# Kernel tuning notes

Measured on AMD Instinct MI355X. Metric: run time of the kernel, lower is better.

## Reference

```python
import jax, jax.numpy as jnp
import numpy as np

N = 100000          # nodes
E = 3200000         # edges (avg degree 32)
IN = 128            # input_dim
H = 16              # hidden1 == hidden2 (GENConv out channels)
OUT = 32            # output_dim
EDGE_DIM = 8        # edge_feature_dim (unused: conv called with edge_attr=None)
MSG_EPS = 1e-7      # GENConv message eps
BN_EPS = 1e-5       # BatchNorm1d eps
T = 1.0             # softmax aggregation temperature


def setup_inputs() -> dict:
    key = jax.random.key(0)
    ks = jax.random.split(key, 24)
    s = lambda fan: 1.0 / np.sqrt(fan)
    inp = {
        "num_nodes": N,
        "edge_index": jax.random.randint(ks[0], (2, E), 0, N, dtype=jnp.int64),
        "edge_attr": jax.random.normal(ks[1], (E, EDGE_DIM), dtype=jnp.float32),
        "x": jax.random.normal(ks[2], (N, IN), dtype=jnp.float32),
        "node_mask": (jnp.arange(N) % 2).astype(jnp.int32),  # exactly N//2 nonzero
        # conv1 lin_src (in != out -> projection)
        "W_src": jax.random.normal(ks[3], (IN, H), dtype=jnp.float32) * s(IN),
        "b_src": jnp.zeros((H,), dtype=jnp.float32),
        # conv1 MLP: [H, 2H, H] with BatchNorm+ReLU between
        "c1_W1": jax.random.normal(ks[4], (H, 2 * H), dtype=jnp.float32) * s(H),
        "c1_b1": jnp.zeros((2 * H,), dtype=jnp.float32),
        "c1_g": jnp.ones((2 * H,), dtype=jnp.float32),
        "c1_be": jnp.zeros((2 * H,), dtype=jnp.float32),
        "c1_W2": jax.random.normal(ks[5], (2 * H, H), dtype=jnp.float32) * s(2 * H),
        "c1_b2": jnp.zeros((H,), dtype=jnp.float32),
        # conv2 MLP (in == out -> no lin_src)
        "c2_W1": jax.random.normal(ks[6], (H, 2 * H), dtype=jnp.float32) * s(H),
        "c2_b1": jnp.zeros((2 * H,), dtype=jnp.float32),
        "c2_g": jnp.ones((2 * H,), dtype=jnp.float32),
        "c2_be": jnp.zeros((2 * H,), dtype=jnp.float32),
        "c2_W2": jax.random.normal(ks[7], (2 * H, H), dtype=jnp.float32) * s(2 * H),
        "c2_b2": jnp.zeros((H,), dtype=jnp.float32),
        # final fc
        "fc_W": jax.random.normal(ks[8], (H, OUT), dtype=jnp.float32) * s(H),
        "fc_b": jnp.zeros((OUT,), dtype=jnp.float32),
    }
    return inp


def _softmax_aggregate(msg, dst, n):
    # per-destination, per-channel softmax-weighted sum (PyG softmax aggr, t=T)
    m = jax.ops.segment_max(msg * T, dst, num_segments=n)          # [n, C]
    ex = jnp.exp(msg * T - m[dst])                                  # [E, C]
    denom = jax.ops.segment_sum(ex, dst, num_segments=n)           # [n, C]
    alpha = ex / denom[dst]
    return jax.ops.segment_sum(alpha * msg, dst, num_segments=n)


def _genconv(x, src, dst, n, lin, mlp):
    if lin is not None:
        x = x @ lin[0] + lin[1]                                     # lin_src projection
    msg = jax.nn.relu(x[src]) + MSG_EPS                             # message (edge_attr=None)
    aggr = _softmax_aggregate(msg, dst, n)
    h = aggr + x                                                    # residual add of x_r
    W1, b1, g, be, W2, b2 = mlp
    h = h @ W1 + b1
    mu = h.mean(axis=0)
    var = h.var(axis=0)                                             # biased var (torch BN)
    h = (h - mu) * jax.lax.rsqrt(var + BN_EPS) * g + be
    return jax.nn.relu(h) @ W2 + b2


def reference(num_nodes, edge_index, edge_attr, x, node_mask,
              W_src, b_src,
              c1_W1, c1_b1, c1_g, c1_be, c1_W2, c1_b2,
              c2_W1, c2_b1, c2_g, c2_be, c2_W2, c2_b2,
              fc_W, fc_b):
    src, dst = edge_index[0], edge_index[1]
    h = _genconv(x, src, dst, num_nodes, (W_src, b_src),
                 (c1_W1, c1_b1, c1_g, c1_be, c1_W2, c1_b2))
    h = jax.nn.relu(h)
    h = _genconv(h, src, dst, num_nodes, None,
                 (c2_W1, c2_b1, c2_g, c2_be, c2_W2, c2_b2))
    h = jax.nn.relu(h)
    out = h @ fc_W + fc_b
    # mask has exactly N//2 nonzeros by construction -> static-size nonzero
    idx = jnp.nonzero(node_mask != 0, size=node_mask.shape[0] // 2)[0]
    return out[idx]
```

## Files before the change

kernel.cpp:

```cpp
#include <hip/hip_runtime.h>

#define NN 100000
#define NE 3200000
#define NB 391
#define NBIN3 782
#define BINW3 128
#define BCAP3 4608
#define BIN_BLOCKS 512
#define CHUNK 6250
#define AGGR4_BLOCKS 1563

static_assert(NB * 256 >= NN, "NB");
static_assert(NBIN3 * BINW3 >= NN, "BINW3");
static_assert(BIN_BLOCKS * CHUNK == NE, "CHUNK");
static_assert(AGGR4_BLOCKS * 256 >= NN * 4, "AGGR4");

__device__ __forceinline__ int wave_incl_scan_i(int v) {
#pragma unroll
  for (int off = 1; off < 64; off <<= 1) {
    int n = __shfl_up(v, off);
    if ((int)(threadIdx.x & 63) >= off) v += n;
  }
  return v;
}

__global__ __launch_bounds__(256) void k_hist(const int* __restrict__ ei,
                                              int* __restrict__ hcnt) {
  __shared__ int hist[NBIN3];
  int t = threadIdx.x;
  for (int i = t; i < NBIN3; i += 256) hist[i] = 0;
  __syncthreads();
  int e0 = blockIdx.x * CHUNK;
  for (int e = e0 + t; e < e0 + CHUNK; e += 256)
    atomicAdd(&hist[ei[NE + e] >> 7], 1);
  __syncthreads();
  for (int i = t; i < NBIN3; i += 256) hcnt[blockIdx.x * NBIN3 + i] = hist[i];
}

__global__ __launch_bounds__(512) void k_hscan(const int* __restrict__ hcnt,
                                               int* __restrict__ hoff,
                                               int* __restrict__ cursor) {
  __shared__ int wsum[8];
  int bin = blockIdx.x;
  int t = threadIdx.x;
  int lane = t & 63, wid = t >> 6;
  int v = hcnt[t * NBIN3 + bin];
  int incl = wave_incl_scan_i(v);
  if (lane == 63) wsum[wid] = incl;
  __syncthreads();
  int base = 0;
  for (int w = 0; w < wid; ++w) base += wsum[w];
  hoff[t * NBIN3 + bin] = base + incl - v;
  if (t == 511) cursor[bin] = base + incl;
}

__global__ __launch_bounds__(256) void k_bin3(const int* __restrict__ ei,
                                              const int* __restrict__ hoff,
                                              unsigned int* __restrict__ binE) {
  __shared__ int run[NBIN3];
  int t = threadIdx.x;
  for (int i = t; i < NBIN3; i += 256) run[i] = hoff[blockIdx.x * NBIN3 + i];
  __syncthreads();
  int e0 = blockIdx.x * CHUNK;
  for (int e = e0 + t; e < e0 + CHUNK; e += 256) {
    int s = ei[e];
    int d = ei[NE + e];
    int bin = d >> 7;
    int slot = atomicAdd(&run[bin], 1);
    binE[(size_t)bin * BCAP3 + slot] = ((unsigned)(d & 127) << 17) | (unsigned)s;
  }
}

__global__ __launch_bounds__(1024) void k_binscan(const int* __restrict__ cursor,
                                                  int* __restrict__ binbase) {
  __shared__ int wsum[16];
  int t = threadIdx.x;
  int v = (t < NBIN3) ? cursor[t] : 0;
  int incl = wave_incl_scan_i(v);
  int lane = t & 63, wid = t >> 6;
  if (lane == 63) wsum[wid] = incl;
  __syncthreads();
  int base = 0;
  for (int w = 0; w < wid; ++w) base += wsum[w];
  if (t < NBIN3) binbase[t] = base + incl - v;
}

__global__ __launch_bounds__(256) void k_csr(const int* __restrict__ cursor,
                                             const int* __restrict__ binbase,
                                             const unsigned int* __restrict__ binE,
                                             int* __restrict__ rowptr,
                                             int* __restrict__ ssrc) {
  __shared__ int cnt[BINW3];
  __shared__ int pex[BINW3];
  __shared__ int run[BINW3];
  __shared__ int w0sum;
  int t = threadIdx.x;
  int bin = blockIdx.x;
  int n = cursor[bin];
  int base = binbase[bin];
  if (t < BINW3) cnt[t] = 0;
  __syncthreads();
  const unsigned int* be = binE + (size_t)bin * BCAP3;
  for (int i = t; i < n; i += 256) atomicAdd(&cnt[be[i] >> 17], 1);
  __syncthreads();
  if (t < BINW3) {
    int v = cnt[t];
    int incl = wave_incl_scan_i(v);
    if (t == 63) w0sum = incl;
    pex[t] = incl - v;
  }
  __syncthreads();
  if (t >= 64 && t < BINW3) pex[t] += w0sum;
  __syncthreads();
  if (t < BINW3) {
    int idx = bin * BINW3 + t;
    if (idx <= NN) rowptr[idx] = base + pex[t];
    run[t] = pex[t];
  }
  __syncthreads();
  for (int i = t; i < n; i += 256) {
    unsigned int v = be[i];
    int dl = (int)(v >> 17);
    int slot = atomicAdd(&run[dl], 1);
    ssrc[base + slot] = (int)(v & 0x1FFFFu);
  }
}

template <bool NONZERO>
__global__ __launch_bounds__(256) void k_block_sum(const int* __restrict__ in, int n,
                                                   int* __restrict__ out) {
  __shared__ int ws[4];
  int i = blockIdx.x * 256 + threadIdx.x;
  int v = 0;
  if (i < n) v = NONZERO ? (in[i] != 0 ? 1 : 0) : in[i];
#pragma unroll
  for (int off = 32; off >= 1; off >>= 1) v += __shfl_down(v, off);
  int lane = threadIdx.x & 63, wid = threadIdx.x >> 6;
  if (lane == 0) ws[wid] = v;
  __syncthreads();
  if (threadIdx.x == 0) out[blockIdx.x] = ws[0] + ws[1] + ws[2] + ws[3];
}

__global__ __launch_bounds__(512) void k_scan_small(const int* __restrict__ in, int n,
                                                    int* __restrict__ out) {
  __shared__ int wsum[8];
  int t = threadIdx.x;
  int v = (t < n) ? in[t] : 0;
  int incl = wave_incl_scan_i(v);
  int lane = t & 63, wid = t >> 6;
  if (lane == 63) wsum[wid] = incl;
  __syncthreads();
  int base = 0;
  for (int w = 0; w < wid; ++w) base += wsum[w];
  if (t < n) out[t] = base + incl - v;
}

__global__ __launch_bounds__(256) void k_lin(const float* __restrict__ x,
                                             const float* __restrict__ Wsrc,
                                             const float* __restrict__ bsrc,
                                             float* __restrict__ A) {
  __shared__ float4 Wl[512];
  __shared__ float bl[16];
  int t = threadIdx.x;
  for (int i = t; i < 512; i += 256) Wl[i] = reinterpret_cast<const float4*>(Wsrc)[i];
  if (t < 16) bl[t] = bsrc[t];
  __syncthreads();
  int node = blockIdx.x * 256 + t;
  if (node >= NN) return;
  float acc[16];
#pragma unroll
  for (int c = 0; c < 16; ++c) acc[c] = bl[c];
  const float4* x4 = reinterpret_cast<const float4*>(x) + (size_t)node * 32;
#pragma unroll 4
  for (int k4 = 0; k4 < 32; ++k4) {
    float4 xv = x4[k4];
    float xs[4];
    xs[0] = xv.x; xs[1] = xv.y; xs[2] = xv.z; xs[3] = xv.w;
#pragma unroll
    for (int j = 0; j < 4; ++j) {
      const float4* wr = &Wl[(k4 * 4 + j) * 4];
      float s = xs[j];
#pragma unroll
      for (int c4 = 0; c4 < 4; ++c4) {
        float4 w = wr[c4];
        acc[c4 * 4 + 0] = fmaf(s, w.x, acc[c4 * 4 + 0]);
        acc[c4 * 4 + 1] = fmaf(s, w.y, acc[c4 * 4 + 1]);
        acc[c4 * 4 + 2] = fmaf(s, w.z, acc[c4 * 4 + 2]);
        acc[c4 * 4 + 3] = fmaf(s, w.w, acc[c4 * 4 + 3]);
      }
    }
  }
  float4* a4 = reinterpret_cast<float4*>(A + (size_t)node * 16);
#pragma unroll
  for (int q = 0; q < 4; ++q)
    a4[q] = make_float4(acc[q * 4], acc[q * 4 + 1], acc[q * 4 + 2], acc[q * 4 + 3]);
}

__global__ __launch_bounds__(256) void k_aggr(const float* __restrict__ Xn,
                                              const int* __restrict__ rowptr,
                                              const int* __restrict__ ssrc,
                                              float* __restrict__ Bout) {
  int gid = blockIdx.x * 256 + threadIdx.x;
  int d = gid >> 2;
  if (d >= NN) return;
  int q = gid & 3;
  int p0 = rowptr[d], p1 = rowptr[d + 1];
  float4 se = make_float4(0.f, 0.f, 0.f, 0.f);
  float4 sm = make_float4(0.f, 0.f, 0.f, 0.f);
  for (int p = p0; p < p1; ++p) {
    int s = ssrc[p];
    float4 v = *reinterpret_cast<const float4*>(Xn + (size_t)s * 16 + q * 4);
    float m0 = (v.x > 0.f ? v.x : 0.f) + 1e-7f;
    float m1 = (v.y > 0.f ? v.y : 0.f) + 1e-7f;
    float m2 = (v.z > 0.f ? v.z : 0.f) + 1e-7f;
    float m3 = (v.w > 0.f ? v.w : 0.f) + 1e-7f;
    float e0 = __expf(m0), e1 = __expf(m1), e2 = __expf(m2), e3 = __expf(m3);
    se.x += e0; se.y += e1; se.z += e2; se.w += e3;
    sm.x = fmaf(e0, m0, sm.x);
    sm.y = fmaf(e1, m1, sm.y);
    sm.z = fmaf(e2, m2, sm.z);
    sm.w = fmaf(e3, m3, sm.w);
  }
  float4 r;
  if (p1 > p0) {
    r.x = sm.x / se.x; r.y = sm.y / se.y; r.z = sm.z / se.z; r.w = sm.w / se.w;
  } else {
    r = make_float4(0.f, 0.f, 0.f, 0.f);
  }
  *reinterpret_cast<float4*>(Bout + (size_t)d * 16 + q * 4) = r;
}

__global__ __launch_bounds__(256) void k_mid(const float* __restrict__ A,
                                             const float* __restrict__ Bv,
                                             const float* __restrict__ W1,
                                             const float* __restrict__ b1,
                                             float* __restrict__ D, float* __restrict__ P) {
  __shared__ float W1l[512];
  __shared__ float b1l[32];
  __shared__ float red[256];
  int t = threadIdx.x;
  for (int i = t; i < 512; i += 256) W1l[i] = W1[i];
  if (t < 32) b1l[t] = b1[t];
  __syncthreads();
  int node = blockIdx.x * 256 + t;
  bool act = node < NN;
  float h[16];
  if (act) {
    const float4* a4 = reinterpret_cast<const float4*>(A + (size_t)node * 16);
    const float4* g4 = reinterpret_cast<const float4*>(Bv + (size_t)node * 16);
#pragma unroll
    for (int q = 0; q < 4; ++q) {
      float4 av = a4[q], gv = g4[q];
      h[q * 4 + 0] = av.x + gv.x;
      h[q * 4 + 1] = av.y + gv.y;
      h[q * 4 + 2] = av.z + gv.z;
      h[q * 4 + 3] = av.w + gv.w;
    }
  } else {
#pragma unroll
    for (int c = 0; c < 16; ++c) h[c] = 0.f;
  }
  float mid[32];
#pragma unroll
  for (int j = 0; j < 32; ++j) mid[j] = b1l[j];
#pragma unroll
  for (int c = 0; c < 16; ++c) {
    float hv = h[c];
    const float4* wr = reinterpret_cast<const float4*>(W1l + c * 32);
#pragma unroll
    for (int j4 = 0; j4 < 8; ++j4) {
      float4 w = wr[j4];
      mid[j4 * 4 + 0] = fmaf(hv, w.x, mid[j4 * 4 + 0]);
      mid[j4 * 4 + 1] = fmaf(hv, w.y, mid[j4 * 4 + 1]);
      mid[j4 * 4 + 2] = fmaf(hv, w.z, mid[j4 * 4 + 2]);
      mid[j4 * 4 + 3] = fmaf(hv, w.w, mid[j4 * 4 + 3]);
    }
  }
  if (act) {
    float4* d4 = reinterpret_cast<float4*>(D + (size_t)node * 32);
#pragma unroll
    for (int j4 = 0; j4 < 8; ++j4)
      d4[j4] = make_float4(mid[j4 * 4], mid[j4 * 4 + 1], mid[j4 * 4 + 2], mid[j4 * 4 + 3]);
  }
  int lane = t & 63, wid = t >> 6;
#pragma unroll
  for (int j = 0; j < 32; ++j) {
    float v = act ? mid[j] : 0.f;
    float v2 = v * v;
#pragma unroll
    for (int off = 32; off >= 1; off >>= 1) {
      v += __shfl_down(v, off);
      v2 += __shfl_down(v2, off);
    }
    if (lane == 0) {
      red[wid * 64 + j] = v;
      red[wid * 64 + 32 + j] = v2;
    }
  }
  __syncthreads();
  if (t < 64) P[blockIdx.x * 64 + t] = red[t] + red[64 + t] + red[128 + t] + red[192 + t];
}

__global__ __launch_bounds__(64) void k_stats(const float* __restrict__ P,
                                              const float* __restrict__ g,
                                              const float* __restrict__ be,
                                              float* __restrict__ SS) {
  __shared__ float s[64];
  int t = threadIdx.x;
  float acc = 0.f;
  for (int b = 0; b < NB; ++b) acc += P[b * 64 + t];
  s[t] = acc;
  __syncthreads();
  if (t < 32) {
    float mu = s[t] * (1.0f / NN);
    float var = s[32 + t] * (1.0f / NN) - mu * mu;
    float sc = g[t] * rsqrtf(var + 1e-5f);
    SS[t] = sc;
    SS[32 + t] = be[t] - mu * sc;
  }
}

__global__ __launch_bounds__(256) void k_out(const float* __restrict__ D,
                                             const float* __restrict__ SS,
                                             const float* __restrict__ W2,
                                             const float* __restrict__ b2,
                                             float* __restrict__ A) {
  __shared__ float W2l[512];
  __shared__ float b2l[16];
  __shared__ float ssl[64];
  int t = threadIdx.x;
  for (int i = t; i < 512; i += 256) W2l[i] = W2[i];
  if (t < 16) b2l[t] = b2[t];
  if (t < 64) ssl[t] = SS[t];
  __syncthreads();
  int node = blockIdx.x * 256 + t;
  if (node >= NN) return;
  float m[32];
  const float4* d4 = reinterpret_cast<const float4*>(D + (size_t)node * 32);
#pragma unroll
  for (int j4 = 0; j4 < 8; ++j4) {
    float4 v = d4[j4];
    m[j4 * 4 + 0] = v.x; m[j4 * 4 + 1] = v.y; m[j4 * 4 + 2] = v.z; m[j4 * 4 + 3] = v.w;
  }
  float o[16];
#pragma unroll
  for (int c = 0; c < 16; ++c) o[c] = b2l[c];
#pragma unroll
  for (int j = 0; j < 32; ++j) {
    float tj = fmaf(m[j], ssl[j], ssl[32 + j]);
    tj = tj > 0.f ? tj : 0.f;
    const float4* wr = reinterpret_cast<const float4*>(W2l + j * 16);
#pragma unroll
    for (int c4 = 0; c4 < 4; ++c4) {
      float4 w = wr[c4];
      o[c4 * 4 + 0] = fmaf(tj, w.x, o[c4 * 4 + 0]);
      o[c4 * 4 + 1] = fmaf(tj, w.y, o[c4 * 4 + 1]);
      o[c4 * 4 + 2] = fmaf(tj, w.z, o[c4 * 4 + 2]);
      o[c4 * 4 + 3] = fmaf(tj, w.w, o[c4 * 4 + 3]);
    }
  }
  float4* a4 = reinterpret_cast<float4*>(A + (size_t)node * 16);
#pragma unroll
  for (int q = 0; q < 4; ++q) {
    float4 r;
    r.x = o[q * 4 + 0] > 0.f ? o[q * 4 + 0] : 0.f;
    r.y = o[q * 4 + 1] > 0.f ? o[q * 4 + 1] : 0.f;
    r.z = o[q * 4 + 2] > 0.f ? o[q * 4 + 2] : 0.f;
    r.w = o[q * 4 + 3] > 0.f ? o[q * 4 + 3] : 0.f;
    a4[q] = r;
  }
}

__global__ __launch_bounds__(256) void k_fc(const float* __restrict__ H2,
                                            const int* __restrict__ mask,
                                            const int* __restrict__ moff,
                                            const float* __restrict__ fcW,
                                            const float* __restrict__ fcb,
                                            float* __restrict__ outp) {
  __shared__ float fwl[512];
  __shared__ float fbl[32];
  __shared__ int ws[4];
  int t = threadIdx.x;
  for (int i = t; i < 512; i += 256) fwl[i] = fcW[i];
  if (t < 32) fbl[t] = fcb[t];
  __syncthreads();
  int node = blockIdx.x * 256 + t;
  int a = (node < NN && mask[node] != 0) ? 1 : 0;
  int incl = wave_incl_scan_i(a);
  int lane = t & 63, wid = t >> 6;
  if (lane == 63) ws[wid] = incl;
  __syncthreads();
  int base = moff[blockIdx.x];
  for (int w = 0; w < wid; ++w) base += ws[w];
  int pos = base + incl - a;
  if (!a) return;
  float h[16];
  const float4* h4 = reinterpret_cast<const float4*>(H2 + (size_t)node * 16);
#pragma unroll
  for (int q = 0; q < 4; ++q) {
    float4 v = h4[q];
    h[q * 4 + 0] = v.x; h[q * 4 + 1] = v.y; h[q * 4 + 2] = v.z; h[q * 4 + 3] = v.w;
  }
  float o[32];
#pragma unroll
  for (int k = 0; k < 32; ++k) o[k] = fbl[k];
#pragma unroll
  for (int c = 0; c < 16; ++c) {
    float hv = h[c];
    const float4* wr = reinterpret_cast<const float4*>(fwl + c * 32);
#pragma unroll
    for (int k4 = 0; k4 < 8; ++k4) {
      float4 w = wr[k4];
      o[k4 * 4 + 0] = fmaf(hv, w.x, o[k4 * 4 + 0]);
      o[k4 * 4 + 1] = fmaf(hv, w.y, o[k4 * 4 + 1]);
      o[k4 * 4 + 2] = fmaf(hv, w.z, o[k4 * 4 + 2]);
      o[k4 * 4 + 3] = fmaf(hv, w.w, o[k4 * 4 + 3]);
    }
  }
  float4* op = reinterpret_cast<float4*>(outp + (size_t)pos * 32);
#pragma unroll
  for (int q = 0; q < 8; ++q)
    op[q] = make_float4(o[q * 4], o[q * 4 + 1], o[q * 4 + 2], o[q * 4 + 3]);
}

extern "C" void kernel_launch(void* const* d_in, const int* in_sizes, int n_in,
                              void* d_out, int out_size, void* d_ws, size_t ws_size,
                              hipStream_t stream) {
  const int* ei = (const int*)d_in[1];
  const float* x = (const float*)d_in[3];
  const int* mask = (const int*)d_in[4];
  const float* Wsrc = (const float*)d_in[5];
  const float* bsrc = (const float*)d_in[6];
  const float* c1W1 = (const float*)d_in[7];
  const float* c1b1 = (const float*)d_in[8];
  const float* c1g = (const float*)d_in[9];
  const float* c1be = (const float*)d_in[10];
  const float* c1W2 = (const float*)d_in[11];
  const float* c1b2 = (const float*)d_in[12];
  const float* c2W1 = (const float*)d_in[13];
  const float* c2b1 = (const float*)d_in[14];
  const float* c2g = (const float*)d_in[15];
  const float* c2be = (const float*)d_in[16];
  const float* c2W2 = (const float*)d_in[17];
  const float* c2b2 = (const float*)d_in[18];
  const float* fcW = (const float*)d_in[19];
  const float* fcb = (const float*)d_in[20];

  char* wp = (char*)d_ws;
  auto nxt = [&](size_t bytes) {
    char* p = wp;
    wp += (bytes + 255) & ~(size_t)255;
    return p;
  };
  float* A = (float*)nxt((size_t)NN * 16 * 4);
  float* Bv = (float*)nxt((size_t)NN * 16 * 4);
  float* D = (float*)nxt((size_t)NN * 32 * 4);
  float* P = (float*)nxt((size_t)NB * 64 * 4);
  float* SS = (float*)nxt(64 * 4);
  int* cursor = (int*)nxt((size_t)NBIN3 * 4);
  int* binbase = (int*)nxt((size_t)NBIN3 * 4);
  unsigned int* binE = (unsigned int*)nxt((size_t)NBIN3 * BCAP3 * 4);
  int* hcnt = (int*)nxt((size_t)BIN_BLOCKS * NBIN3 * 4);
  int* hoff = (int*)nxt((size_t)BIN_BLOCKS * NBIN3 * 4);
  int* rowptr = (int*)nxt((size_t)(NN + 1) * 4);
  int* ssrc = (int*)nxt((size_t)NE * 4);
  int* mcnt = (int*)nxt((size_t)NB * 4);
  int* moff = (int*)nxt((size_t)NB * 4);

  k_hist<<<BIN_BLOCKS, 256, 0, stream>>>(ei, hcnt);
  k_hscan<<<NBIN3, 512, 0, stream>>>(hcnt, hoff, cursor);
  k_bin3<<<BIN_BLOCKS, 256, 0, stream>>>(ei, hoff, binE);
  k_binscan<<<1, 1024, 0, stream>>>(cursor, binbase);
  k_csr<<<NBIN3, 256, 0, stream>>>(cursor, binbase, binE, rowptr, ssrc);

  k_lin<<<NB, 256, 0, stream>>>(x, Wsrc, bsrc, A);
  k_aggr<<<AGGR4_BLOCKS, 256, 0, stream>>>(A, rowptr, ssrc, Bv);
  k_mid<<<NB, 256, 0, stream>>>(A, Bv, c1W1, c1b1, D, P);
  k_stats<<<1, 64, 0, stream>>>(P, c1g, c1be, SS);
  k_out<<<NB, 256, 0, stream>>>(D, SS, c1W2, c1b2, A);

  k_aggr<<<AGGR4_BLOCKS, 256, 0, stream>>>(A, rowptr, ssrc, Bv);
  k_mid<<<NB, 256, 0, stream>>>(A, Bv, c2W1, c2b1, D, P);
  k_stats<<<1, 64, 0, stream>>>(P, c2g, c2be, SS);
  k_out<<<NB, 256, 0, stream>>>(D, SS, c2W2, c2b2, A);

  k_block_sum<true><<<NB, 256, 0, stream>>>(mask, NN, mcnt);
  k_scan_small<<<1, 512, 0, stream>>>(mcnt, NB, moff);
  k_fc<<<NB, 256, 0, stream>>>(A, mask, moff, fcW, fcb, (float*)d_out);
}
```

Measured before the change: 516.0 us.

## Split node features into two 8-channel planes and aggregate each plane separately

```diff
diff --git a/kernel.cpp b/kernel.cpp
--- a/kernel.cpp
+++ b/kernel.cpp
@@ -6,14 +6,14 @@
 #define NBIN3 782
 #define BINW3 128
 #define BCAP3 4608
-#define BIN_BLOCKS 512
-#define CHUNK 6250
-#define AGGR4_BLOCKS 1563
+#define BIN_BLOCKS 256
+#define CHUNK 12500
+#define AGGR2_BLOCKS 782
 
 static_assert(NB * 256 >= NN, "NB");
 static_assert(NBIN3 * BINW3 >= NN, "BINW3");
 static_assert(BIN_BLOCKS * CHUNK == NE, "CHUNK");
-static_assert(AGGR4_BLOCKS * 256 >= NN * 4, "AGGR4");
+static_assert(AGGR2_BLOCKS * 256 >= NN * 2, "AGGR2");
 
 __device__ __forceinline__ int wave_incl_scan_i(int v) {
 #pragma unroll
@@ -37,10 +37,10 @@
   for (int i = t; i < NBIN3; i += 256) hcnt[blockIdx.x * NBIN3 + i] = hist[i];
 }
 
-__global__ __launch_bounds__(512) void k_hscan(const int* __restrict__ hcnt,
+__global__ __launch_bounds__(256) void k_hscan(const int* __restrict__ hcnt,
                                                int* __restrict__ hoff,
                                                int* __restrict__ cursor) {
-  __shared__ int wsum[8];
+  __shared__ int wsum[4];
   int bin = blockIdx.x;
   int t = threadIdx.x;
   int lane = t & 63, wid = t >> 6;
@@ -51,7 +51,7 @@
   int base = 0;
   for (int w = 0; w < wid; ++w) base += wsum[w];
   hoff[t * NBIN3 + bin] = base + incl - v;
-  if (t == 511) cursor[bin] = base + incl;
+  if (t == 255) cursor[bin] = base + incl;
 }
 
 __global__ __launch_bounds__(256) void k_bin3(const int* __restrict__ ei,
@@ -158,7 +158,8 @@
 __global__ __launch_bounds__(256) void k_lin(const float* __restrict__ x,
                                              const float* __restrict__ Wsrc,
                                              const float* __restrict__ bsrc,
-                                             float* __restrict__ A) {
+                                             float* __restrict__ A0,
+                                             float* __restrict__ A1) {
   __shared__ float4 Wl[512];
   __shared__ float bl[16];
   int t = threadIdx.x;
@@ -190,26 +191,28 @@
       }
     }
   }
-  float4* a4 = reinterpret_cast<float4*>(A + (size_t)node * 16);
-#pragma unroll
-  for (int q = 0; q < 4; ++q)
-    a4[q] = make_float4(acc[q * 4], acc[q * 4 + 1], acc[q * 4 + 2], acc[q * 4 + 3]);
-}
-
-__global__ __launch_bounds__(256) void k_aggr(const float* __restrict__ Xn,
+  float4* a0 = reinterpret_cast<float4*>(A0 + (size_t)node * 8);
+  float4* a1 = reinterpret_cast<float4*>(A1 + (size_t)node * 8);
+  a0[0] = make_float4(acc[0], acc[1], acc[2], acc[3]);
+  a0[1] = make_float4(acc[4], acc[5], acc[6], acc[7]);
+  a1[0] = make_float4(acc[8], acc[9], acc[10], acc[11]);
+  a1[1] = make_float4(acc[12], acc[13], acc[14], acc[15]);
+}
+
+__global__ __launch_bounds__(256) void k_aggr(const float* __restrict__ Xp,
                                               const int* __restrict__ rowptr,
                                               const int* __restrict__ ssrc,
-                                              float* __restrict__ Bout) {
+                                              float* __restrict__ Bp) {
   int gid = blockIdx.x * 256 + threadIdx.x;
-  int d = gid >> 2;
+  int d = gid >> 1;
   if (d >= NN) return;
-  int q = gid & 3;
+  int q = gid & 1;
   int p0 = rowptr[d], p1 = rowptr[d + 1];
   float4 se = make_float4(0.f, 0.f, 0.f, 0.f);
   float4 sm = make_float4(0.f, 0.f, 0.f, 0.f);
   for (int p = p0; p < p1; ++p) {
     int s = ssrc[p];
-    float4 v = *reinterpret_cast<const float4*>(Xn + (size_t)s * 16 + q * 4);
+    float4 v = *reinterpret_cast<const float4*>(Xp + (size_t)s * 8 + q * 4);
     float m0 = (v.x > 0.f ? v.x : 0.f) + 1e-7f;
     float m1 = (v.y > 0.f ? v.y : 0.f) + 1e-7f;
     float m2 = (v.z > 0.f ? v.z : 0.f) + 1e-7f;
@@ -227,11 +230,13 @@
   } else {
     r = make_float4(0.f, 0.f, 0.f, 0.f);
   }
-  *reinterpret_cast<float4*>(Bout + (size_t)d * 16 + q * 4) = r;
-}
-
-__global__ __launch_bounds__(256) void k_mid(const float* __restrict__ A,
-                                             const float* __restrict__ Bv,
+  *reinterpret_cast<float4*>(Bp + (size_t)d * 8 + q * 4) = r;
+}
+
+__global__ __launch_bounds__(256) void k_mid(const float* __restrict__ A0,
+                                             const float* __restrict__ A1,
+                                             const float* __restrict__ Bv0,
+                                             const float* __restrict__ Bv1,
                                              const float* __restrict__ W1,
                                              const float* __restrict__ b1,
                                              float* __restrict__ D, float* __restrict__ P) {
@@ -246,15 +251,25 @@
   bool act = node < NN;
   float h[16];
   if (act) {
-    const float4* a4 = reinterpret_cast<const float4*>(A + (size_t)node * 16);
-    const float4* g4 = reinterpret_cast<const float4*>(Bv + (size_t)node * 16);
-#pragma unroll
-    for (int q = 0; q < 4; ++q) {
-      float4 av = a4[q], gv = g4[q];
+    const float4* a0 = reinterpret_cast<const float4*>(A0 + (size_t)node * 8);
+    const float4* a1 = reinterpret_cast<const float4*>(A1 + (size_t)node * 8);
+    const float4* g0 = reinterpret_cast<const float4*>(Bv0 + (size_t)node * 8);
+    const float4* g1 = reinterpret_cast<const float4*>(Bv1 + (size_t)node * 8);
+#pragma unroll
+    for (int q = 0; q < 2; ++q) {
+      float4 av = a0[q], gv = g0[q];
       h[q * 4 + 0] = av.x + gv.x;
       h[q * 4 + 1] = av.y + gv.y;
       h[q * 4 + 2] = av.z + gv.z;
       h[q * 4 + 3] = av.w + gv.w;
+    }
+#pragma unroll
+    for (int q = 0; q < 2; ++q) {
+      float4 av = a1[q], gv = g1[q];
+      h[8 + q * 4 + 0] = av.x + gv.x;
+      h[8 + q * 4 + 1] = av.y + gv.y;
+      h[8 + q * 4 + 2] = av.z + gv.z;
+      h[8 + q * 4 + 3] = av.w + gv.w;
     }
   } else {
 #pragma unroll
@@ -324,7 +339,8 @@
                                              const float* __restrict__ SS,
                                              const float* __restrict__ W2,
                                              const float* __restrict__ b2,
-                                             float* __restrict__ A) {
+                                             float* __restrict__ A0,
+                                             float* __restrict__ A1) {
   __shared__ float W2l[512];
   __shared__ float b2l[16];
   __shared__ float ssl[64];
@@ -359,19 +375,18 @@
       o[c4 * 4 + 3] = fmaf(tj, w.w, o[c4 * 4 + 3]);
     }
   }
-  float4* a4 = reinterpret_cast<float4*>(A + (size_t)node * 16);
-#pragma unroll
-  for (int q = 0; q < 4; ++q) {
-    float4 r;
-    r.x = o[q * 4 + 0] > 0.f ? o[q * 4 + 0] : 0.f;
-    r.y = o[q * 4 + 1] > 0.f ? o[q * 4 + 1] : 0.f;
-    r.z = o[q * 4 + 2] > 0.f ? o[q * 4 + 2] : 0.f;
-    r.w = o[q * 4 + 3] > 0.f ? o[q * 4 + 3] : 0.f;
-    a4[q] = r;
-  }
-}
-
-__global__ __launch_bounds__(256) void k_fc(const float* __restrict__ H2,
+#pragma unroll
+  for (int c = 0; c < 16; ++c) o[c] = o[c] > 0.f ? o[c] : 0.f;
+  float4* a0 = reinterpret_cast<float4*>(A0 + (size_t)node * 8);
+  float4* a1 = reinterpret_cast<float4*>(A1 + (size_t)node * 8);
+  a0[0] = make_float4(o[0], o[1], o[2], o[3]);
+  a0[1] = make_float4(o[4], o[5], o[6], o[7]);
+  a1[0] = make_float4(o[8], o[9], o[10], o[11]);
+  a1[1] = make_float4(o[12], o[13], o[14], o[15]);
+}
+
+__global__ __launch_bounds__(256) void k_fc(const float* __restrict__ A0,
+                                            const float* __restrict__ A1,
                                             const int* __restrict__ mask,
                                             const int* __restrict__ moff,
                                             const float* __restrict__ fcW,
@@ -395,11 +410,17 @@
   int pos = base + incl - a;
   if (!a) return;
   float h[16];
-  const float4* h4 = reinterpret_cast<const float4*>(H2 + (size_t)node * 16);
-#pragma unroll
-  for (int q = 0; q < 4; ++q) {
-    float4 v = h4[q];
+  const float4* h0 = reinterpret_cast<const float4*>(A0 + (size_t)node * 8);
+  const float4* h1 = reinterpret_cast<const float4*>(A1 + (size_t)node * 8);
+#pragma unroll
+  for (int q = 0; q < 2; ++q) {
+    float4 v = h0[q];
     h[q * 4 + 0] = v.x; h[q * 4 + 1] = v.y; h[q * 4 + 2] = v.z; h[q * 4 + 3] = v.w;
+  }
+#pragma unroll
+  for (int q = 0; q < 2; ++q) {
+    float4 v = h1[q];
+    h[8 + q * 4 + 0] = v.x; h[8 + q * 4 + 1] = v.y; h[8 + q * 4 + 2] = v.z; h[8 + q * 4 + 3] = v.w;
   }
   float o[32];
 #pragma unroll
@@ -452,8 +473,10 @@
     wp += (bytes + 255) & ~(size_t)255;
     return p;
   };
-  float* A = (float*)nxt((size_t)NN * 16 * 4);
-  float* Bv = (float*)nxt((size_t)NN * 16 * 4);
+  float* A0 = (float*)nxt((size_t)NN * 8 * 4);
+  float* A1 = (float*)nxt((size_t)NN * 8 * 4);
+  float* Bv0 = (float*)nxt((size_t)NN * 8 * 4);
+  float* Bv1 = (float*)nxt((size_t)NN * 8 * 4);
   float* D = (float*)nxt((size_t)NN * 32 * 4);
   float* P = (float*)nxt((size_t)NB * 64 * 4);
   float* SS = (float*)nxt(64 * 4);
@@ -468,23 +491,25 @@
   int* moff = (int*)nxt((size_t)NB * 4);
 
   k_hist<<<BIN_BLOCKS, 256, 0, stream>>>(ei, hcnt);
-  k_hscan<<<NBIN3, 512, 0, stream>>>(hcnt, hoff, cursor);
+  k_hscan<<<NBIN3, 256, 0, stream>>>(hcnt, hoff, cursor);
   k_bin3<<<BIN_BLOCKS, 256, 0, stream>>>(ei, hoff, binE);
   k_binscan<<<1, 1024, 0, stream>>>(cursor, binbase);
   k_csr<<<NBIN3, 256, 0, stream>>>(cursor, binbase, binE, rowptr, ssrc);
 
-  k_lin<<<NB, 256, 0, stream>>>(x, Wsrc, bsrc, A);
-  k_aggr<<<AGGR4_BLOCKS, 256, 0, stream>>>(A, rowptr, ssrc, Bv);
-  k_mid<<<NB, 256, 0, stream>>>(A, Bv, c1W1, c1b1, D, P);
+  k_lin<<<NB, 256, 0, stream>>>(x, Wsrc, bsrc, A0, A1);
+  k_aggr<<<AGGR2_BLOCKS, 256, 0, stream>>>(A0, rowptr, ssrc, Bv0);
+  k_aggr<<<AGGR2_BLOCKS, 256, 0, stream>>>(A1, rowptr, ssrc, Bv1);
+  k_mid<<<NB, 256, 0, stream>>>(A0, A1, Bv0, Bv1, c1W1, c1b1, D, P);
   k_stats<<<1, 64, 0, stream>>>(P, c1g, c1be, SS);
-  k_out<<<NB, 256, 0, stream>>>(D, SS, c1W2, c1b2, A);
-
-  k_aggr<<<AGGR4_BLOCKS, 256, 0, stream>>>(A, rowptr, ssrc, Bv);
-  k_mid<<<NB, 256, 0, stream>>>(A, Bv, c2W1, c2b1, D, P);
+  k_out<<<NB, 256, 0, stream>>>(D, SS, c1W2, c1b2, A0, A1);
+
+  k_aggr<<<AGGR2_BLOCKS, 256, 0, stream>>>(A0, rowptr, ssrc, Bv0);
+  k_aggr<<<AGGR2_BLOCKS, 256, 0, stream>>>(A1, rowptr, ssrc, Bv1);
+  k_mid<<<NB, 256, 0, stream>>>(A0, A1, Bv0, Bv1, c2W1, c2b1, D, P);
   k_stats<<<1, 64, 0, stream>>>(P, c2g, c2be, SS);
-  k_out<<<NB, 256, 0, stream>>>(D, SS, c2W2, c2b2, A);
+  k_out<<<NB, 256, 0, stream>>>(D, SS, c2W2, c2b2, A0, A1);
 
   k_block_sum<true><<<NB, 256, 0, stream>>>(mask, NN, mcnt);
   k_scan_small<<<1, 512, 0, stream>>>(mcnt, NB, moff);
-  k_fc<<<NB, 256, 0, stream>>>(A, mask, moff, fcW, fcb, (float*)d_out);
-}
+  k_fc<<<NB, 256, 0, stream>>>(A0, A1, mask, moff, fcW, fcb, (float*)d_out);
+}
```

After: 604.7 us. 1.17x slower.
